# Performance work log

Measured on AMD Instinct MI355X. Metric: run time of the kernel, lower is better.

The kernel has to match this reference:

```python
import jax, jax.numpy as jnp
import numpy as np

N_NODES = 100000


def setup_inputs() -> dict:
    key = jax.random.key(0)
    k1, k2, k3 = jax.random.split(key, 3)
    x = jax.random.normal(k1, (N_NODES, 128), dtype=jnp.float32)
    edge_index = jax.random.randint(k2, (2, 1600000), 0, N_NODES, dtype=jnp.int64)
    # GCNConv linear weight (hidden, input) and bias; PReLU slope (init 0.25 as in torch)
    W = jax.random.normal(k3, (128, 128), dtype=jnp.float32) * (1.0 / np.sqrt(128))
    b = jnp.zeros((128,), dtype=jnp.float32)
    prelu_a = jnp.full((1,), 0.25, dtype=jnp.float32)
    return {"x": x, "edge_index": edge_index, "W": W, "b": b, "prelu_a": prelu_a}


def reference(x, edge_index, W, b, prelu_a):
    n = x.shape[0]
    # add self loops (as in forward's add_self_loops)
    loop = jnp.arange(n, dtype=edge_index.dtype)
    src = jnp.concatenate([edge_index[0], loop])  # [E+N]
    dst = jnp.concatenate([edge_index[1], loop])
    # linear transform first (small GEMM), then gather/scatter on hidden dim
    h = x @ W.T  # [N, H]
    # symmetric degree normalization 1/sqrt(deg_src * deg_dst), deg = in-degree incl. self-loop
    ones = jnp.ones_like(dst, dtype=h.dtype)
    deg = jax.ops.segment_sum(ones, dst, num_segments=n)
    dinv = jnp.where(deg > 0, jax.lax.rsqrt(deg), 0.0)  # [N]
    norm = dinv[src] * dinv[dst]  # [E+N]
    msg = h[src] * norm[:, None]  # gather + scale, memory-bound
    out = jax.ops.segment_sum(msg, dst, num_segments=n) + b  # scatter-add
    # PReLU (single shared slope); dropout is identity in eval mode
    out = jnp.where(out >= 0, out, prelu_a[0] * out)
    return out
```

## Files before the change

### kernel.cpp

```cpp
#include <hip/hip_runtime.h>
#include <math.h>

#define HDIM 128
#define BSH 8
#define LSH 24
#define CH 4096
#define GEMM_BLKS 256
#define GSPLIT 160

typedef __attribute__((ext_vector_type(8))) short short8;
typedef __attribute__((ext_vector_type(4))) float f32x4;

__device__ inline unsigned short bf16_hi(float f) {
    return (unsigned short)(__float_as_uint(f) >> 16);
}
__device__ inline unsigned short bf16_rn(float f) {
    unsigned int u = __float_as_uint(f);
    return (unsigned short)((u + 0x7FFF + ((u >> 16) & 1)) >> 16);
}

__global__ __launch_bounds__(256) void prep_kernel(
    const float* __restrict__ W, uint4* __restrict__ Whg, uint4* __restrict__ Wlg) {
    const int t = threadIdx.x;
    for (int idx = t; idx < 2048; idx += 256) {
        const int j = idx >> 4;
        const int c = idx & 15;
        const float4* wp = (const float4*)(W + (size_t)j * HDIM + c * 8);
        float4 va = wp[0], vb = wp[1];
        float vs[8] = {va.x, va.y, va.z, va.w, vb.x, vb.y, vb.z, vb.w};
        unsigned short h[8], l[8];
        #pragma unroll
        for (int k = 0; k < 8; ++k) {
            h[k] = bf16_hi(vs[k]);
            float hf = __uint_as_float((unsigned int)h[k] << 16);
            l[k] = bf16_hi(vs[k] - hf);
        }
        uint4 hch, lch;
        hch.x = (unsigned int)h[0] | ((unsigned int)h[1] << 16);
        hch.y = (unsigned int)h[2] | ((unsigned int)h[3] << 16);
        hch.z = (unsigned int)h[4] | ((unsigned int)h[5] << 16);
        hch.w = (unsigned int)h[6] | ((unsigned int)h[7] << 16);
        lch.x = (unsigned int)l[0] | ((unsigned int)l[1] << 16);
        lch.y = (unsigned int)l[2] | ((unsigned int)l[3] << 16);
        lch.z = (unsigned int)l[4] | ((unsigned int)l[5] << 16);
        lch.w = (unsigned int)l[6] | ((unsigned int)l[7] << 16);
        Whg[idx] = hch;
        Wlg[idx] = lch;
    }
}

__device__ __forceinline__ void gemm_body(
    const float* __restrict__ x, const uint4* __restrict__ Whg,
    const uint4* __restrict__ Wlg, unsigned short* __restrict__ gb, int n,
    int g0, int g1, int bid, int nblk) {
    const int t = threadIdx.x;
    const int wave = t >> 6;
    const int lane = t & 63;
    const int q = lane >> 4;
    const int m = lane & 15;

    for (int grp = g0 + bid; grp < g1; grp += nblk) {
        const int rowbase = (grp << 7) + (wave << 5);

        f32x4 acc[2][8];
        #pragma unroll
        for (int mt = 0; mt < 2; ++mt)
            #pragma unroll
            for (int ct = 0; ct < 8; ++ct)
                acc[mt][ct] = (f32x4){0.f, 0.f, 0.f, 0.f};

        #pragma unroll
        for (int kk = 0; kk < 4; ++kk) {
            short8 ah[2], al[2];
            #pragma unroll
            for (int mt = 0; mt < 2; ++mt) {
                const int r = rowbase + (mt << 4) + m;
                float vs[8];
                if (r < n) {
                    const float4* xp = (const float4*)(x + (size_t)r * HDIM + (kk << 5) + (q << 3));
                    float4 va = xp[0], vb = xp[1];
                    vs[0] = va.x; vs[1] = va.y; vs[2] = va.z; vs[3] = va.w;
                    vs[4] = vb.x; vs[5] = vb.y; vs[6] = vb.z; vs[7] = vb.w;
                } else {
                    #pragma unroll
                    for (int k = 0; k < 8; ++k) vs[k] = 0.f;
                }
                #pragma unroll
                for (int k = 0; k < 8; ++k) {
                    unsigned short h = bf16_hi(vs[k]);
                    float hf = __uint_as_float((unsigned int)h << 16);
                    unsigned short lo = bf16_hi(vs[k] - hf);
                    ah[mt][k] = (short)h;
                    al[mt][k] = (short)lo;
                }
            }
            #pragma unroll
            for (int ct = 0; ct < 8; ++ct) {
                const int nn = (ct << 4) + m;
                const int fidx = (nn << 4) | ((kk << 2) + q);
                short8 bh = *(const short8*)&Whg[fidx];
                short8 bl = *(const short8*)&Wlg[fidx];
                #pragma unroll
                for (int mt = 0; mt < 2; ++mt) {
                    acc[mt][ct] = __builtin_amdgcn_mfma_f32_16x16x32_bf16(ah[mt], bh, acc[mt][ct], 0, 0, 0);
                    acc[mt][ct] = __builtin_amdgcn_mfma_f32_16x16x32_bf16(al[mt], bh, acc[mt][ct], 0, 0, 0);
                    acc[mt][ct] = __builtin_amdgcn_mfma_f32_16x16x32_bf16(ah[mt], bl, acc[mt][ct], 0, 0, 0);
                }
            }
        }

        #pragma unroll
        for (int mt = 0; mt < 2; ++mt) {
            #pragma unroll
            for (int rr = 0; rr < 4; ++rr) {
                const int grow = rowbase + (mt << 4) + (q << 2) + rr;
                if (grow < n) {
                    unsigned short* gp = gb + (size_t)grow * HDIM + m;
                    #pragma unroll
                    for (int ct = 0; ct < 8; ++ct)
                        gp[ct << 4] = bf16_rn(acc[mt][ct][rr]);
                }
            }
        }
    }
}

__device__ __forceinline__ void binA_body(
    const int* __restrict__ dst, int E, int* __restrict__ bcnt,
    int chunk, int* hist) {
    const int t = threadIdx.x;
    const int c0 = chunk * CH;
    hist[t] = 0;
    hist[t + 256] = 0;
    __syncthreads();
    #pragma unroll
    for (int k = 0; k < CH / 256; ++k) {
        int e = c0 + t + (k << 8);
        if (e < E) atomicAdd(&hist[dst[e] >> BSH], 1);
    }
    __syncthreads();
    if (hist[t] > 0) atomicAdd(&bcnt[t], hist[t]);
    if (hist[t + 256] > 0) atomicAdd(&bcnt[t + 256], hist[t + 256]);
}

__device__ __forceinline__ void binB_body(
    const int* __restrict__ ei, int E, const int* __restrict__ bcnt,
    int* __restrict__ boff, unsigned int* __restrict__ eb,
    int chunk, int* hist, int* bb, int* base, int* cur, int NB) {
    const int t = threadIdx.x;
    const int c0 = chunk * CH;
    hist[t] = 0;
    hist[t + 256] = 0;
    __syncthreads();

    int sv[CH / 256], dv[CH / 256];
    #pragma unroll
    for (int k = 0; k < CH / 256; ++k) {
        int e = c0 + t + (k << 8);
        if (e < E) {
            sv[k] = ei[e];
            dv[k] = ei[E + e];
            atomicAdd(&hist[dv[k] >> BSH], 1);
        } else {
            dv[k] = -1;
        }
    }
    __syncthreads();

    if (t < 64) {
        int carry = 0;
        #pragma unroll
        for (int c = 0; c < 512; c += 64) {
            int idx = c + t;
            int v = (idx < NB) ? bcnt[idx] : 0;
            int xs = v;
            #pragma unroll
            for (int off = 1; off < 64; off <<= 1) {
                int u = __shfl_up(xs, off);
                if (t >= off) xs += u;
            }
            bb[idx] = carry + xs - v;
            carry += __shfl(xs, 63);
        }
    }
    __syncthreads();

    if (hist[t] > 0)       base[t]       = bb[t]       + atomicAdd(&boff[t],       hist[t]);
    if (hist[t + 256] > 0) base[t + 256] = bb[t + 256] + atomicAdd(&boff[t + 256], hist[t + 256]);
    cur[t] = 0;
    cur[t + 256] = 0;
    __syncthreads();

    #pragma unroll
    for (int k = 0; k < CH / 256; ++k) {
        if (dv[k] >= 0) {
            int bkt = dv[k] >> BSH;
            int o = atomicAdd(&cur[bkt], 1);
            eb[(size_t)base[bkt] + o] =
                ((unsigned int)(dv[k] & ((1 << BSH) - 1)) << LSH) | (unsigned int)sv[k];
        }
    }
}

__global__ __launch_bounds__(256) void fuse1_kernel(
    const int* __restrict__ dst, int E, int* __restrict__ bcnt,
    const float* __restrict__ x, const uint4* __restrict__ Whg,
    const uint4* __restrict__ Wlg, unsigned short* __restrict__ gb, int n) {
    __shared__ int s_a[512];
    const int bid = blockIdx.x;
    if (bid < GEMM_BLKS)
        gemm_body(x, Whg, Wlg, gb, n, 0, GSPLIT, bid, GEMM_BLKS);
    else
        binA_body(dst, E, bcnt, bid - GEMM_BLKS, s_a);
}

__global__ __launch_bounds__(256) void fuse2_kernel(
    const int* __restrict__ ei, int E, const int* __restrict__ bcnt,
    int* __restrict__ boff, unsigned int* __restrict__ eb,
    const float* __restrict__ x, const uint4* __restrict__ Whg,
    const uint4* __restrict__ Wlg, unsigned short* __restrict__ gb,
    int n, int ngroups, int NB) {
    __shared__ int s_h[512], s_bb[512], s_ba[512], s_cu[512];
    const int bid = blockIdx.x;
    if (bid < GEMM_BLKS)
        gemm_body(x, Whg, Wlg, gb, n, GSPLIT, ngroups, bid, GEMM_BLKS);
    else
        binB_body(ei, E, bcnt, boff, eb, bid - GEMM_BLKS, s_h, s_bb, s_ba, s_cu, NB);
}

__global__ __launch_bounds__(256) void binC_kernel(
    const unsigned int* __restrict__ eb, const int* __restrict__ bcnt,
    int* __restrict__ row_ptr, float* __restrict__ dinv,
    int* __restrict__ col, int n, int NB) {
    __shared__ int hist[256];
    __shared__ int cur[256];
    __shared__ int red[256];
    __shared__ int wsum[4];
    const int t = threadIdx.x;
    const int b = blockIdx.x;
    const int node0 = b << BSH;

    int part = 0;
    for (int k = t; k < b; k += 256) part += bcnt[k];
    red[t] = part;
    __syncthreads();
    #pragma unroll
    for (int off = 128; off > 0; off >>= 1) {
        if (t < off) red[t] += red[t + off];
        __syncthreads();
    }
    const int e0 = red[0];
    const int e1 = e0 + bcnt[b];

    hist[t] = 0;
    __syncthreads();
    for (int e = e0 + t; e < e1; e += 256)
        atomicAdd(&hist[eb[e] >> LSH], 1);
    __syncthreads();
    const int v = hist[t];
    int x = v;
    #pragma unroll
    for (int off = 1; off < 64; off <<= 1) {
        int u = __shfl_up(x, off);
        if ((t & 63) >= off) x += u;
    }
    if ((t & 63) == 63) wsum[t >> 6] = x;
    __syncthreads();
    if (t < 4) {
        int y = wsum[t];
        #pragma unroll
        for (int off = 1; off < 4; off <<= 1) {
            int u = __shfl_up(y, off);
            if (t >= off) y += u;
        }
        wsum[t] = y;
    }
    __syncthreads();
    int excl = x - v + ((t >> 6) ? wsum[(t >> 6) - 1] : 0);

    int node = node0 + t;
    if (node < n) {
        row_ptr[node] = e0 + excl;
        dinv[node] = rsqrtf((float)v + 1.0f);
        if (node == n - 1) row_ptr[n] = e0 + excl + v;
    }
    cur[t] = e0 + excl;
    __syncthreads();
    for (int e = e0 + t; e < e1; e += 256) {
        unsigned int p = eb[e];
        int pos = atomicAdd(&cur[p >> LSH], 1);
        col[pos] = (int)(p & ((1u << LSH) - 1));
    }
}

#define EDGE_ACC(d, u) \
    a[0] = fmaf(d, __uint_as_float((u).x << 16), a[0]); \
    a[1] = fmaf(d, __uint_as_float((u).x & 0xffff0000u), a[1]); \
    a[2] = fmaf(d, __uint_as_float((u).y << 16), a[2]); \
    a[3] = fmaf(d, __uint_as_float((u).y & 0xffff0000u), a[3]); \
    a[4] = fmaf(d, __uint_as_float((u).z << 16), a[4]); \
    a[5] = fmaf(d, __uint_as_float((u).z & 0xffff0000u), a[5]); \
    a[6] = fmaf(d, __uint_as_float((u).w << 16), a[6]); \
    a[7] = fmaf(d, __uint_as_float((u).w & 0xffff0000u), a[7]);

__global__ __launch_bounds__(256) void gather_kernel(
    const int* __restrict__ row_ptr, const int* __restrict__ col,
    const uint4* __restrict__ gbr, const float* __restrict__ dinv,
    const float* __restrict__ bias, const float* __restrict__ prelu_a,
    float* __restrict__ out, int n) {
    const int wv = threadIdx.x >> 6;
    const int lane = threadIdx.x & 63;
    const int q = lane >> 4;
    const int l16 = lane & 15;
    const int i = blockIdx.x * 4 + wv;
    if (i >= n) return;

    const int beg = row_ptr[i];
    const int end = row_ptr[i + 1];
    const float di = dinv[i];

    float a[8];
    #pragma unroll
    for (int k = 0; k < 8; ++k) a[k] = 0.f;

    if (q == 0) {
        uint4 u = gbr[(size_t)i * 16 + l16];
        EDGE_ACC(di, u)
    }

    int e = beg + q;
    for (; e + 12 < end; e += 16) {
        int s0 = col[e];
        int s1 = col[e + 4];
        int s2 = col[e + 8];
        int s3 = col[e + 12];
        float d0 = dinv[s0], d1 = dinv[s1], d2 = dinv[s2], d3 = dinv[s3];
        uint4 u0 = gbr[(size_t)s0 * 16 + l16];
        uint4 u1 = gbr[(size_t)s1 * 16 + l16];
        uint4 u2 = gbr[(size_t)s2 * 16 + l16];
        uint4 u3 = gbr[(size_t)s3 * 16 + l16];
        EDGE_ACC(d0, u0)
        EDGE_ACC(d1, u1)
        EDGE_ACC(d2, u2)
        EDGE_ACC(d3, u3)
    }
    for (; e + 4 < end; e += 8) {
        int s0 = col[e];
        int s1 = col[e + 4];
        float d0 = dinv[s0], d1 = dinv[s1];
        uint4 u0 = gbr[(size_t)s0 * 16 + l16];
        uint4 u1 = gbr[(size_t)s1 * 16 + l16];
        EDGE_ACC(d0, u0)
        EDGE_ACC(d1, u1)
    }
    if (e < end) {
        int s = col[e];
        float d = dinv[s];
        uint4 u = gbr[(size_t)s * 16 + l16];
        EDGE_ACC(d, u)
    }

    #pragma unroll
    for (int k = 0; k < 8; ++k) {
        a[k] += __shfl_xor(a[k], 16);
        a[k] += __shfl_xor(a[k], 32);
    }

    const float aa = prelu_a[0];
    const int c0 = (l16 << 3) + (q << 1);
    float2 bb = *(const float2*)(bias + c0);
    float v0 = di * a[(q << 1) + 0] + bb.x;
    float v1 = di * a[(q << 1) + 1] + bb.y;
    v0 = v0 >= 0.f ? v0 : aa * v0;
    v1 = v1 >= 0.f ? v1 : aa * v1;
    *(float2*)(out + (size_t)i * HDIM + c0) = make_float2(v0, v1);
}

extern "C" void kernel_launch(void* const* d_in, const int* in_sizes, int n_in,
                              void* d_out, int out_size, void* d_ws, size_t ws_size,
                              hipStream_t stream) {
    const float* x  = (const float*)d_in[0];
    const int*   ei = (const int*)d_in[1];
    const float* W  = (const float*)d_in[2];
    const float* b  = (const float*)d_in[3];
    const float* pa = (const float*)d_in[4];

    const int n = in_sizes[0] / HDIM;
    const int E = in_sizes[1] / 2;
    const int NB = (n + (1 << BSH) - 1) >> BSH;
    const int ngroups = (n + 127) >> 7;

    float* out = (float*)d_out;

    unsigned short* gb      = (unsigned short*)d_ws;
    unsigned int*   eb      = (unsigned int*)(gb + (size_t)n * HDIM);
    uint4*          Whg     = (uint4*)(eb + (size_t)E);
    uint4*          Wlg     = Whg + 2048;
    float*          dinv    = (float*)(Wlg + 2048);
    int*            row_ptr = (int*)(dinv + n);
    int*            col     = row_ptr + (n + 1);
    int*            bcnt    = col + E;
    int*            boff    = bcnt + 512;

    hipMemsetAsync(bcnt, 0, 1024 * sizeof(int), stream);

    const int nchunk = (E + CH - 1) / CH;
    prep_kernel<<<1, 256, 0, stream>>>(W, Whg, Wlg);
    fuse1_kernel<<<GEMM_BLKS + nchunk, 256, 0, stream>>>(ei + E, E, bcnt, x, Whg, Wlg, gb, n);
    fuse2_kernel<<<GEMM_BLKS + nchunk, 256, 0, stream>>>(ei, E, bcnt, boff, eb, x, Whg, Wlg, gb, n, ngroups, NB);
    binC_kernel<<<NB, 256, 0, stream>>>(eb, bcnt, row_ptr, dinv, col, n, NB);
    gather_kernel<<<(n + 3) / 4, 256, 0, stream>>>(row_ptr, col, (const uint4*)gb, dinv, b, pa, out, n);
}
```

Before: 258.7 us.

## Replace bucketed two-pass CSR build with global-atomic degree count and direct fill

Replaces the three-stage bucket sort (per-chunk shared histograms, bucketed edge staging buffer, per-bucket local sort) with a direct CSR build: global atomic in-degree count fused with the full GEMM, a block-sum and scan for row pointers, then a fill pass that atomically claims slots per destination node. This drops the intermediate packed-edge buffer and one full pass over the edges, and the GEMM now runs in a single launch instead of being split. In exchange it relies on heavily contended global atomics over many addresses, produces a nondeterministic neighbour order within each row, and adds more small launches plus a memset of the degree array.

```diff
diff --git a/kernel.cpp b/kernel.cpp
--- a/kernel.cpp
+++ b/kernel.cpp
@@ -3,10 +3,9 @@
 
 #define HDIM 128
 #define BSH 8
-#define LSH 24
-#define CH 4096
 #define GEMM_BLKS 256
-#define GSPLIT 160
+#define HIST_BLKS 128
+#define FILL_BLKS 512
 
 typedef __attribute__((ext_vector_type(8))) short short8;
 typedef __attribute__((ext_vector_type(4))) float f32x4;
@@ -125,139 +124,54 @@
     }
 }
 
-__device__ __forceinline__ void binA_body(
-    const int* __restrict__ dst, int E, int* __restrict__ bcnt,
-    int chunk, int* hist) {
-    const int t = threadIdx.x;
-    const int c0 = chunk * CH;
-    hist[t] = 0;
-    hist[t + 256] = 0;
-    __syncthreads();
-    #pragma unroll
-    for (int k = 0; k < CH / 256; ++k) {
-        int e = c0 + t + (k << 8);
-        if (e < E) atomicAdd(&hist[dst[e] >> BSH], 1);
-    }
-    __syncthreads();
-    if (hist[t] > 0) atomicAdd(&bcnt[t], hist[t]);
-    if (hist[t + 256] > 0) atomicAdd(&bcnt[t + 256], hist[t + 256]);
-}
-
-__device__ __forceinline__ void binB_body(
-    const int* __restrict__ ei, int E, const int* __restrict__ bcnt,
-    int* __restrict__ boff, unsigned int* __restrict__ eb,
-    int chunk, int* hist, int* bb, int* base, int* cur, int NB) {
-    const int t = threadIdx.x;
-    const int c0 = chunk * CH;
-    hist[t] = 0;
-    hist[t + 256] = 0;
-    __syncthreads();
-
-    int sv[CH / 256], dv[CH / 256];
-    #pragma unroll
-    for (int k = 0; k < CH / 256; ++k) {
-        int e = c0 + t + (k << 8);
-        if (e < E) {
-            sv[k] = ei[e];
-            dv[k] = ei[E + e];
-            atomicAdd(&hist[dv[k] >> BSH], 1);
-        } else {
-            dv[k] = -1;
-        }
-    }
-    __syncthreads();
-
-    if (t < 64) {
-        int carry = 0;
-        #pragma unroll
-        for (int c = 0; c < 512; c += 64) {
-            int idx = c + t;
-            int v = (idx < NB) ? bcnt[idx] : 0;
-            int xs = v;
-            #pragma unroll
-            for (int off = 1; off < 64; off <<= 1) {
-                int u = __shfl_up(xs, off);
-                if (t >= off) xs += u;
-            }
-            bb[idx] = carry + xs - v;
-            carry += __shfl(xs, 63);
-        }
-    }
-    __syncthreads();
-
-    if (hist[t] > 0)       base[t]       = bb[t]       + atomicAdd(&boff[t],       hist[t]);
-    if (hist[t + 256] > 0) base[t + 256] = bb[t + 256] + atomicAdd(&boff[t + 256], hist[t + 256]);
-    cur[t] = 0;
-    cur[t + 256] = 0;
-    __syncthreads();
-
-    #pragma unroll
-    for (int k = 0; k < CH / 256; ++k) {
-        if (dv[k] >= 0) {
-            int bkt = dv[k] >> BSH;
-            int o = atomicAdd(&cur[bkt], 1);
-            eb[(size_t)base[bkt] + o] =
-                ((unsigned int)(dv[k] & ((1 << BSH) - 1)) << LSH) | (unsigned int)sv[k];
-        }
-    }
-}
-
-__global__ __launch_bounds__(256) void fuse1_kernel(
-    const int* __restrict__ dst, int E, int* __restrict__ bcnt,
-    const float* __restrict__ x, const uint4* __restrict__ Whg,
-    const uint4* __restrict__ Wlg, unsigned short* __restrict__ gb, int n) {
-    __shared__ int s_a[512];
-    const int bid = blockIdx.x;
-    if (bid < GEMM_BLKS)
-        gemm_body(x, Whg, Wlg, gb, n, 0, GSPLIT, bid, GEMM_BLKS);
-    else
-        binA_body(dst, E, bcnt, bid - GEMM_BLKS, s_a);
-}
-
-__global__ __launch_bounds__(256) void fuse2_kernel(
-    const int* __restrict__ ei, int E, const int* __restrict__ bcnt,
-    int* __restrict__ boff, unsigned int* __restrict__ eb,
+__global__ __launch_bounds__(256) void fuseA_kernel(
+    const int* __restrict__ ei, int E, int* __restrict__ deg,
     const float* __restrict__ x, const uint4* __restrict__ Whg,
     const uint4* __restrict__ Wlg, unsigned short* __restrict__ gb,
-    int n, int ngroups, int NB) {
-    __shared__ int s_h[512], s_bb[512], s_ba[512], s_cu[512];
+    int n, int ngroups) {
     const int bid = blockIdx.x;
-    if (bid < GEMM_BLKS)
-        gemm_body(x, Whg, Wlg, gb, n, GSPLIT, ngroups, bid, GEMM_BLKS);
-    else
-        binB_body(ei, E, bcnt, boff, eb, bid - GEMM_BLKS, s_h, s_bb, s_ba, s_cu, NB);
-}
-
-__global__ __launch_bounds__(256) void binC_kernel(
-    const unsigned int* __restrict__ eb, const int* __restrict__ bcnt,
-    int* __restrict__ row_ptr, float* __restrict__ dinv,
-    int* __restrict__ col, int n, int NB) {
-    __shared__ int hist[256];
-    __shared__ int cur[256];
+    if (bid < GEMM_BLKS) {
+        gemm_body(x, Whg, Wlg, gb, n, 0, ngroups, bid, GEMM_BLKS);
+    } else {
+        const int t = threadIdx.x;
+        const int hb = bid - GEMM_BLKS;
+        const int* __restrict__ dstp = ei + E;
+        const int stride = HIST_BLKS * 256 * 4;
+        for (int e = (hb * 256 + t) * 4; e + 3 < E; e += stride) {
+            int4 d = *(const int4*)(dstp + e);
+            atomicAdd(&deg[d.x], 1);
+            atomicAdd(&deg[d.y], 1);
+            atomicAdd(&deg[d.z], 1);
+            atomicAdd(&deg[d.w], 1);
+        }
+        if (hb == 0) {
+            for (int e = (E & ~3) + t; e < E; e += 256)
+                atomicAdd(&deg[dstp[e]], 1);
+        }
+    }
+}
+
+__global__ __launch_bounds__(256) void bsum_kernel(
+    const int* __restrict__ deg, int* __restrict__ bsum, int n) {
     __shared__ int red[256];
-    __shared__ int wsum[4];
     const int t = threadIdx.x;
     const int b = blockIdx.x;
-    const int node0 = b << BSH;
-
-    int part = 0;
-    for (int k = t; k < b; k += 256) part += bcnt[k];
-    red[t] = part;
+    const int node = (b << BSH) + t;
+    red[t] = (node < n) ? deg[node] : 0;
     __syncthreads();
     #pragma unroll
     for (int off = 128; off > 0; off >>= 1) {
         if (t < off) red[t] += red[t + off];
         __syncthreads();
     }
-    const int e0 = red[0];
-    const int e1 = e0 + bcnt[b];
-
-    hist[t] = 0;
-    __syncthreads();
-    for (int e = e0 + t; e < e1; e += 256)
-        atomicAdd(&hist[eb[e] >> LSH], 1);
-    __syncthreads();
-    const int v = hist[t];
+    if (t == 0) bsum[b] = red[0];
+}
+
+__global__ __launch_bounds__(512) void scan_kernel(
+    const int* __restrict__ bsum, int* __restrict__ bbase, int NB, int E) {
+    __shared__ int wsum[8];
+    const int t = threadIdx.x;
+    const int v = (t < NB) ? bsum[t] : 0;
     int x = v;
     #pragma unroll
     for (int off = 1; off < 64; off <<= 1) {
@@ -266,6 +180,38 @@
     }
     if ((t & 63) == 63) wsum[t >> 6] = x;
     __syncthreads();
+    if (t < 8) {
+        int y = wsum[t];
+        #pragma unroll
+        for (int off = 1; off < 8; off <<= 1) {
+            int u = __shfl_up(y, off);
+            if (t >= off) y += u;
+        }
+        wsum[t] = y;
+    }
+    __syncthreads();
+    int excl = x - v + ((t >> 6) ? wsum[(t >> 6) - 1] : 0);
+    if (t < NB) bbase[t] = excl;
+    if (t == NB - 1) bbase[NB] = excl + v;
+}
+
+__global__ __launch_bounds__(256) void rowptr_kernel(
+    const int* __restrict__ deg, const int* __restrict__ bbase,
+    int* __restrict__ row_ptr, int* __restrict__ cur,
+    float* __restrict__ dinv, int n) {
+    __shared__ int wsum[4];
+    const int t = threadIdx.x;
+    const int b = blockIdx.x;
+    const int node = (b << BSH) + t;
+    const int v = (node < n) ? deg[node] : 0;
+    int x = v;
+    #pragma unroll
+    for (int off = 1; off < 64; off <<= 1) {
+        int u = __shfl_up(x, off);
+        if ((t & 63) >= off) x += u;
+    }
+    if ((t & 63) == 63) wsum[t >> 6] = x;
+    __syncthreads();
     if (t < 4) {
         int y = wsum[t];
         #pragma unroll
@@ -276,20 +222,41 @@
         wsum[t] = y;
     }
     __syncthreads();
-    int excl = x - v + ((t >> 6) ? wsum[(t >> 6) - 1] : 0);
-
-    int node = node0 + t;
+    const int excl = x - v + ((t >> 6) ? wsum[(t >> 6) - 1] : 0);
     if (node < n) {
-        row_ptr[node] = e0 + excl;
+        const int base = bbase[b] + excl;
+        row_ptr[node] = base;
+        cur[node] = base;
         dinv[node] = rsqrtf((float)v + 1.0f);
-        if (node == n - 1) row_ptr[n] = e0 + excl + v;
-    }
-    cur[t] = e0 + excl;
-    __syncthreads();
-    for (int e = e0 + t; e < e1; e += 256) {
-        unsigned int p = eb[e];
-        int pos = atomicAdd(&cur[p >> LSH], 1);
-        col[pos] = (int)(p & ((1u << LSH) - 1));
+        if (node == n - 1) row_ptr[n] = base + v;
+    }
+}
+
+__global__ __launch_bounds__(256) void fill_kernel(
+    const int* __restrict__ ei, int E, int* __restrict__ cur,
+    int* __restrict__ col) {
+    const int t = threadIdx.x;
+    const int fb = blockIdx.x;
+    const int* __restrict__ srcp = ei;
+    const int* __restrict__ dstp = ei + E;
+    const int stride = FILL_BLKS * 256 * 4;
+    for (int e = (fb * 256 + t) * 4; e + 3 < E; e += stride) {
+        int4 s = *(const int4*)(srcp + e);
+        int4 d = *(const int4*)(dstp + e);
+        int p0 = atomicAdd(&cur[d.x], 1);
+        int p1 = atomicAdd(&cur[d.y], 1);
+        int p2 = atomicAdd(&cur[d.z], 1);
+        int p3 = atomicAdd(&cur[d.w], 1);
+        col[p0] = s.x;
+        col[p1] = s.y;
+        col[p2] = s.z;
+        col[p3] = s.w;
+    }
+    if (fb == 0) {
+        for (int e = (E & ~3) + t; e < E; e += 256) {
+            int p = atomicAdd(&cur[dstp[e]], 1);
+            col[p] = srcp[e];
+        }
     }
 }
 
@@ -393,21 +360,23 @@
     float* out = (float*)d_out;
 
     unsigned short* gb      = (unsigned short*)d_ws;
-    unsigned int*   eb      = (unsigned int*)(gb + (size_t)n * HDIM);
-    uint4*          Whg     = (uint4*)(eb + (size_t)E);
+    uint4*          Whg     = (uint4*)(gb + (size_t)n * HDIM);
     uint4*          Wlg     = Whg + 2048;
-    float*          dinv    = (float*)(Wlg + 2048);
-    int*            row_ptr = (int*)(dinv + n);
-    int*            col     = row_ptr + (n + 1);
-    int*            bcnt    = col + E;
-    int*            boff    = bcnt + 512;
-
-    hipMemsetAsync(bcnt, 0, 1024 * sizeof(int), stream);
-
-    const int nchunk = (E + CH - 1) / CH;
+    int*            deg     = (int*)(Wlg + 2048);
+    int*            row_ptr = deg + n;
+    int*            cur     = row_ptr + (n + 1);
+    float*          dinv    = (float*)(cur + n);
+    int*            col     = (int*)(dinv + n);
+    int*            bsum    = col + E;
+    int*            bbase   = bsum + 512;
+
+    hipMemsetAsync(deg, 0, (size_t)n * sizeof(int), stream);
+
     prep_kernel<<<1, 256, 0, stream>>>(W, Whg, Wlg);
-    fuse1_kernel<<<GEMM_BLKS + nchunk, 256, 0, stream>>>(ei + E, E, bcnt, x, Whg, Wlg, gb, n);
-    fuse2_kernel<<<GEMM_BLKS + nchunk, 256, 0, stream>>>(ei, E, bcnt, boff, eb, x, Whg, Wlg, gb, n, ngroups, NB);
-    binC_kernel<<<NB, 256, 0, stream>>>(eb, bcnt, row_ptr, dinv, col, n, NB);
+    fuseA_kernel<<<GEMM_BLKS + HIST_BLKS, 256, 0, stream>>>(ei, E, deg, x, Whg, Wlg, gb, n, ngroups);
+    bsum_kernel<<<NB, 256, 0, stream>>>(deg, bsum, n);
+    scan_kernel<<<1, 512, 0, stream>>>(bsum, bbase, NB, E);
+    rowptr_kernel<<<NB, 256, 0, stream>>>(deg, bbase, row_ptr, cur, dinv, n);
+    fill_kernel<<<FILL_BLKS, 256, 0, stream>>>(ei, E, cur, col);
     gather_kernel<<<(n + 3) / 4, 256, 0, stream>>>(row_ptr, col, (const uint4*)gb, dinv, b, pa, out, n);
 }
```

New measurement: 384.9 us. 48.8% more time.

## Use 512-node buckets, smaller GEMM tiles, and occupancy hints

Applied to the files above, without the earlier changes.

Bucket width grows from 256 to 512 nodes, which halves the bucket count to about 196 and lets the binning histograms use 256-entry arrays. binC now runs 512 threads per bucket to match. The GEMM tile shrinks to 64 rows per block with one 16-row MFMA tile per wave, and the GEMM split point moves to rebalance work between the two fused kernels. Launch bounds request 4 blocks per CU, aiming for higher occupancy and lower register pressure at the cost of less reuse of W per loaded tile.

```diff
diff --git a/kernel.cpp b/kernel.cpp
--- a/kernel.cpp
+++ b/kernel.cpp
@@ -2,11 +2,11 @@
 #include <math.h>
 
 #define HDIM 128
-#define BSH 8
-#define LSH 24
+#define BSH 9
+#define LSH 23
 #define CH 4096
 #define GEMM_BLKS 256
-#define GSPLIT 160
+#define GSPLIT 800
 
 typedef __attribute__((ext_vector_type(8))) short short8;
 typedef __attribute__((ext_vector_type(4))) float f32x4;
@@ -60,21 +60,18 @@
     const int m = lane & 15;
 
     for (int grp = g0 + bid; grp < g1; grp += nblk) {
-        const int rowbase = (grp << 7) + (wave << 5);
-
-        f32x4 acc[2][8];
-        #pragma unroll
-        for (int mt = 0; mt < 2; ++mt)
-            #pragma unroll
-            for (int ct = 0; ct < 8; ++ct)
-                acc[mt][ct] = (f32x4){0.f, 0.f, 0.f, 0.f};
+        const int rowbase = (grp << 6) + (wave << 4);
+
+        f32x4 acc[8];
+        #pragma unroll
+        for (int ct = 0; ct < 8; ++ct)
+            acc[ct] = (f32x4){0.f, 0.f, 0.f, 0.f};
 
         #pragma unroll
         for (int kk = 0; kk < 4; ++kk) {
-            short8 ah[2], al[2];
-            #pragma unroll
-            for (int mt = 0; mt < 2; ++mt) {
-                const int r = rowbase + (mt << 4) + m;
+            short8 ah, al;
+            {
+                const int r = rowbase + m;
                 float vs[8];
                 if (r < n) {
                     const float4* xp = (const float4*)(x + (size_t)r * HDIM + (kk << 5) + (q << 3));
@@ -90,8 +87,8 @@
                     unsigned short h = bf16_hi(vs[k]);
                     float hf = __uint_as_float((unsigned int)h << 16);
                     unsigned short lo = bf16_hi(vs[k] - hf);
-                    ah[mt][k] = (short)h;
-                    al[mt][k] = (short)lo;
+                    ah[k] = (short)h;
+                    al[k] = (short)lo;
                 }
             }
             #pragma unroll
@@ -100,26 +97,20 @@
                 const int fidx = (nn << 4) | ((kk << 2) + q);
                 short8 bh = *(const short8*)&Whg[fidx];
                 short8 bl = *(const short8*)&Wlg[fidx];
+                acc[ct] = __builtin_amdgcn_mfma_f32_16x16x32_bf16(ah, bh, acc[ct], 0, 0, 0);
+                acc[ct] = __builtin_amdgcn_mfma_f32_16x16x32_bf16(al, bh, acc[ct], 0, 0, 0);
+                acc[ct] = __builtin_amdgcn_mfma_f32_16x16x32_bf16(ah, bl, acc[ct], 0, 0, 0);
+            }
+        }
+
+        #pragma unroll
+        for (int rr = 0; rr < 4; ++rr) {
+            const int grow = rowbase + (q << 2) + rr;
+            if (grow < n) {
+                unsigned short* gp = gb + (size_t)grow * HDIM + m;
                 #pragma unroll
-                for (int mt = 0; mt < 2; ++mt) {
-                    acc[mt][ct] = __builtin_amdgcn_mfma_f32_16x16x32_bf16(ah[mt], bh, acc[mt][ct], 0, 0, 0);
-                    acc[mt][ct] = __builtin_amdgcn_mfma_f32_16x16x32_bf16(al[mt], bh, acc[mt][ct], 0, 0, 0);
-                    acc[mt][ct] = __builtin_amdgcn_mfma_f32_16x16x32_bf16(ah[mt], bl, acc[mt][ct], 0, 0, 0);
-                }
-            }
-        }
-
-        #pragma unroll
-        for (int mt = 0; mt < 2; ++mt) {
-            #pragma unroll
-            for (int rr = 0; rr < 4; ++rr) {
-                const int grow = rowbase + (mt << 4) + (q << 2) + rr;
-                if (grow < n) {
-                    unsigned short* gp = gb + (size_t)grow * HDIM + m;
-                    #pragma unroll
-                    for (int ct = 0; ct < 8; ++ct)
-                        gp[ct << 4] = bf16_rn(acc[mt][ct][rr]);
-                }
+                for (int ct = 0; ct < 8; ++ct)
+                    gp[ct << 4] = bf16_rn(acc[ct][rr]);
             }
         }
     }
@@ -131,7 +122,6 @@
     const int t = threadIdx.x;
     const int c0 = chunk * CH;
     hist[t] = 0;
-    hist[t + 256] = 0;
     __syncthreads();
     #pragma unroll
     for (int k = 0; k < CH / 256; ++k) {
@@ -140,7 +130,6 @@
     }
     __syncthreads();
     if (hist[t] > 0) atomicAdd(&bcnt[t], hist[t]);
-    if (hist[t + 256] > 0) atomicAdd(&bcnt[t + 256], hist[t + 256]);
 }
 
 __device__ __forceinline__ void binB_body(
@@ -150,7 +139,6 @@
     const int t = threadIdx.x;
     const int c0 = chunk * CH;
     hist[t] = 0;
-    hist[t + 256] = 0;
     __syncthreads();
 
     int sv[CH / 256], dv[CH / 256];
@@ -170,7 +158,7 @@
     if (t < 64) {
         int carry = 0;
         #pragma unroll
-        for (int c = 0; c < 512; c += 64) {
+        for (int c = 0; c < 256; c += 64) {
             int idx = c + t;
             int v = (idx < NB) ? bcnt[idx] : 0;
             int xs = v;
@@ -185,10 +173,8 @@
     }
     __syncthreads();
 
-    if (hist[t] > 0)       base[t]       = bb[t]       + atomicAdd(&boff[t],       hist[t]);
-    if (hist[t + 256] > 0) base[t + 256] = bb[t + 256] + atomicAdd(&boff[t + 256], hist[t + 256]);
+    if (hist[t] > 0) base[t] = bb[t] + atomicAdd(&boff[t], hist[t]);
     cur[t] = 0;
-    cur[t + 256] = 0;
     __syncthreads();
 
     #pragma unroll
@@ -202,11 +188,11 @@
     }
 }
 
-__global__ __launch_bounds__(256) void fuse1_kernel(
+__global__ __launch_bounds__(256, 4) void fuse1_kernel(
     const int* __restrict__ dst, int E, int* __restrict__ bcnt,
     const float* __restrict__ x, const uint4* __restrict__ Whg,
     const uint4* __restrict__ Wlg, unsigned short* __restrict__ gb, int n) {
-    __shared__ int s_a[512];
+    __shared__ int s_a[256];
     const int bid = blockIdx.x;
     if (bid < GEMM_BLKS)
         gemm_body(x, Whg, Wlg, gb, n, 0, GSPLIT, bid, GEMM_BLKS);
@@ -214,13 +200,13 @@
         binA_body(dst, E, bcnt, bid - GEMM_BLKS, s_a);
 }
 
-__global__ __launch_bounds__(256) void fuse2_kernel(
+__global__ __launch_bounds__(256, 4) void fuse2_kernel(
     const int* __restrict__ ei, int E, const int* __restrict__ bcnt,
     int* __restrict__ boff, unsigned int* __restrict__ eb,
     const float* __restrict__ x, const uint4* __restrict__ Whg,
     const uint4* __restrict__ Wlg, unsigned short* __restrict__ gb,
     int n, int ngroups, int NB) {
-    __shared__ int s_h[512], s_bb[512], s_ba[512], s_cu[512];
+    __shared__ int s_h[256], s_bb[256], s_ba[256], s_cu[256];
     const int bid = blockIdx.x;
     if (bid < GEMM_BLKS)
         gemm_body(x, Whg, Wlg, gb, n, GSPLIT, ngroups, bid, GEMM_BLKS);
@@ -228,24 +214,24 @@
         binB_body(ei, E, bcnt, boff, eb, bid - GEMM_BLKS, s_h, s_bb, s_ba, s_cu, NB);
 }
 
-__global__ __launch_bounds__(256) void binC_kernel(
+__global__ __launch_bounds__(512) void binC_kernel(
     const unsigned int* __restrict__ eb, const int* __restrict__ bcnt,
     int* __restrict__ row_ptr, float* __restrict__ dinv,
     int* __restrict__ col, int n, int NB) {
-    __shared__ int hist[256];
-    __shared__ int cur[256];
-    __shared__ int red[256];
-    __shared__ int wsum[4];
+    __shared__ int hist[512];
+    __shared__ int cur[512];
+    __shared__ int red[512];
+    __shared__ int wsum[8];
     const int t = threadIdx.x;
     const int b = blockIdx.x;
     const int node0 = b << BSH;
 
     int part = 0;
-    for (int k = t; k < b; k += 256) part += bcnt[k];
+    for (int k = t; k < b; k += 512) part += bcnt[k];
     red[t] = part;
     __syncthreads();
     #pragma unroll
-    for (int off = 128; off > 0; off >>= 1) {
+    for (int off = 256; off > 0; off >>= 1) {
         if (t < off) red[t] += red[t + off];
         __syncthreads();
     }
@@ -254,7 +240,7 @@
 
     hist[t] = 0;
     __syncthreads();
-    for (int e = e0 + t; e < e1; e += 256)
+    for (int e = e0 + t; e < e1; e += 512)
         atomicAdd(&hist[eb[e] >> LSH], 1);
     __syncthreads();
     const int v = hist[t];
@@ -266,10 +252,10 @@
     }
     if ((t & 63) == 63) wsum[t >> 6] = x;
     __syncthreads();
-    if (t < 4) {
+    if (t < 8) {
         int y = wsum[t];
         #pragma unroll
-        for (int off = 1; off < 4; off <<= 1) {
+        for (int off = 1; off < 8; off <<= 1) {
             int u = __shfl_up(y, off);
             if (t >= off) y += u;
         }
@@ -286,7 +272,7 @@
     }
     cur[t] = e0 + excl;
     __syncthreads();
-    for (int e = e0 + t; e < e1; e += 256) {
+    for (int e = e0 + t; e < e1; e += 512) {
         unsigned int p = eb[e];
         int pos = atomicAdd(&cur[p >> LSH], 1);
         col[pos] = (int)(p & ((1u << LSH) - 1));
@@ -388,7 +374,7 @@
     const int n = in_sizes[0] / HDIM;
     const int E = in_sizes[1] / 2;
     const int NB = (n + (1 << BSH) - 1) >> BSH;
-    const int ngroups = (n + 127) >> 7;
+    const int ngroups = (n + 63) >> 6;
 
     float* out = (float*)d_out;
 
@@ -400,14 +386,14 @@
     int*            row_ptr = (int*)(dinv + n);
     int*            col     = row_ptr + (n + 1);
     int*            bcnt    = col + E;
-    int*            boff    = bcnt + 512;
-
-    hipMemsetAsync(bcnt, 0, 1024 * sizeof(int), stream);
+    int*            boff    = bcnt + 256;
+
+    hipMemsetAsync(bcnt, 0, 512 * sizeof(int), stream);
 
     const int nchunk = (E + CH - 1) / CH;
     prep_kernel<<<1, 256, 0, stream>>>(W, Whg, Wlg);
     fuse1_kernel<<<GEMM_BLKS + nchunk, 256, 0, stream>>>(ei + E, E, bcnt, x, Whg, Wlg, gb, n);
     fuse2_kernel<<<GEMM_BLKS + nchunk, 256, 0, stream>>>(ei, E, bcnt, boff, eb, x, Whg, Wlg, gb, n, ngroups, NB);
-    binC_kernel<<<NB, 256, 0, stream>>>(eb, bcnt, row_ptr, dinv, col, n, NB);
+    binC_kernel<<<NB, 512, 0, stream>>>(eb, bcnt, row_ptr, dinv, col, n, NB);
     gather_kernel<<<(n + 3) / 4, 256, 0, stream>>>(row_ptr, col, (const uint4*)gb, dinv, b, pa, out, n);
 }
```

Measured after the change: 348.7 us. 1.35x slower.
